# Optimization experiments

Hardware: AMD Instinct MI355X
Metric: run time of the kernel (lower is better)

The kernel has to match this reference:

```python
import jax, jax.numpy as jnp
import numpy as np

B, C, FS, Z_DIM, OUT_C, F_SIZE = 256, 512, 16, 64, 1, 3
NZ = FS * FS  # 256


def setup_inputs() -> dict:
    key = jax.random.key(0)
    k1, k2, k3, k4, k5 = jax.random.split(key, 5)
    # z: [B, C, H, W]
    z = jax.random.normal(k1, (B, C, FS, FS), dtype=jnp.float32)
    # 512 independent per-channel Linear(Nz -> z_dim): stacked weights/biases
    lim_in = 1.0 / np.sqrt(NZ)
    W_in = jax.random.uniform(k2, (C, NZ, Z_DIM), minval=-lim_in, maxval=lim_in, dtype=jnp.float32)
    b_in = jax.random.uniform(k3, (C, Z_DIM), minval=-lim_in, maxval=lim_in, dtype=jnp.float32)
    # shared Linear(z_dim -> out_channels*f_size*f_size)
    lim_out = 1.0 / np.sqrt(Z_DIM)
    W_out = jax.random.uniform(k4, (Z_DIM, OUT_C * F_SIZE * F_SIZE), minval=-lim_out, maxval=lim_out, dtype=jnp.float32)
    b_out = jax.random.uniform(k5, (OUT_C * F_SIZE * F_SIZE,), minval=-lim_out, maxval=lim_out, dtype=jnp.float32)
    return {"z": z, "W_in": W_in, "b_in": b_in, "W_out": W_out, "b_out": b_out}


def reference(z, W_in, b_in, W_out, b_out):
    batch = z.shape[0]
    # flatten each channel's HxW map: [B, C, Nz]
    x = z.reshape(batch, C, NZ)
    # per-channel Linear as one batched GEMM: [B, C, z_dim]
    a = jnp.einsum('bcn,cnz->bcz', x, W_in) + b_in[None, :, :]
    # shared output Linear: [B, C, out_c*f*f]
    k = jnp.einsum('bcz,zk->bck', a, W_out) + b_out
    # [B, C, out_channels, f_size, f_size]
    return k.reshape(batch, C, OUT_C, F_SIZE, F_SIZE)
```

## Files before the change

kernel.cpp:

```cpp
#include <hip/hip_runtime.h>

#define BB 256
#define CC 512
#define NZ 256
#define ZD 64
#define KK 9

template<int CTRL>
__device__ __forceinline__ float dpp_add(float v) {
    int o = __builtin_amdgcn_update_dpp(0, __float_as_int(v), CTRL, 0xF, 0xF, true);
    return v + __int_as_float(o);
}
__device__ __forceinline__ float red8(float v) {
    v = dpp_add<0xB1>(v);
    v = dpp_add<0x4E>(v);
    v = dpp_add<0x141>(v);
    return v;
}

__global__ __launch_bounds__(512, 2)
void hyper_kernel(const float* __restrict__ z,
                  const float* __restrict__ W_in,
                  const float* __restrict__ b_in,
                  const float* __restrict__ W_out,
                  const float* __restrict__ b_out,
                  float* __restrict__ out) {
    __shared__ __align__(16) float s_wfT[KK * NZ];
    __shared__ __align__(16) float s_woutT[KK * ZD];
    __shared__ float s_bin[ZD];
    __shared__ float s_biask[KK];

    const int c = blockIdx.x;
    const int t = threadIdx.x;

    for (int i = t; i < KK * ZD; i += 512) {
        float v = W_out[i];
        int zz = i / KK, k = i - zz * KK;
        s_woutT[k * ZD + zz] = v;
    }
    if (t < ZD) s_bin[t] = b_in[c * ZD + t];
    __syncthreads();

    {
        const int n = t >> 1, half = t & 1;
        const float* wrow = W_in + ((size_t)c * NZ + n) * ZD + half * 32;
        float acc[KK];
#pragma unroll
        for (int k = 0; k < KK; ++k) acc[k] = 0.f;
#pragma unroll
        for (int j = 0; j < 8; ++j) {
            const float4 w = *reinterpret_cast<const float4*>(wrow + 4 * j);
#pragma unroll
            for (int k = 0; k < KK; ++k) {
                const float4 wo = *reinterpret_cast<const float4*>(
                    &s_woutT[k * ZD + half * 32 + 4 * j]);
                acc[k] += w.x * wo.x + w.y * wo.y + w.z * wo.z + w.w * wo.w;
            }
        }
#pragma unroll
        for (int k = 0; k < KK; ++k) acc[k] = dpp_add<0xB1>(acc[k]);
        if (half == 0) {
#pragma unroll
            for (int k = 0; k < KK; ++k) s_wfT[k * NZ + n] = acc[k];
        }
        if (t < KK) {
            float s = 0.f;
            for (int zz = 0; zz < ZD; ++zz) s += s_bin[zz] * s_woutT[t * ZD + zz];
            s_biask[t] = s + b_out[t];
        }
    }
    __syncthreads();

    const int lane = t & 63;
    const int wave = t >> 6;
    const int g = lane >> 3;
    const int sub = lane & 7;
    const int b0 = wave * 32 + g * 4;
    const float biasS = s_biask[sub];
    const float bias8 = s_biask[8];

    const float* xp = z + ((size_t)b0 * CC + c) * NZ + sub * 4;
    const size_t bstr = (size_t)CC * NZ;

    float acc[4][KK];
#pragma unroll
    for (int bb = 0; bb < 4; ++bb)
#pragma unroll
        for (int k = 0; k < KK; ++k) acc[bb][k] = 0.f;

    float4 xb[2][4];
#pragma unroll
    for (int bb = 0; bb < 4; ++bb)
        xb[0][bb] = *reinterpret_cast<const float4*>(xp + bb * bstr);

#pragma unroll
    for (int j = 0; j < 8; ++j) {
        if (j < 7) {
#pragma unroll
            for (int bb = 0; bb < 4; ++bb)
                xb[(j + 1) & 1][bb] =
                    *reinterpret_cast<const float4*>(xp + bb * bstr + (j + 1) * 32);
        }
#pragma unroll
        for (int k = 0; k < KK; ++k) {
            const float4 wf = *reinterpret_cast<const float4*>(
                &s_wfT[k * NZ + sub * 4 + j * 32]);
#pragma unroll
            for (int bb = 0; bb < 4; ++bb) {
                const float4 x = xb[j & 1][bb];
                acc[bb][k] += x.x * wf.x + x.y * wf.y + x.z * wf.z + x.w * wf.w;
            }
        }
    }

#pragma unroll
    for (int bb = 0; bb < 4; ++bb)
#pragma unroll
        for (int k = 0; k < KK; ++k) acc[bb][k] = red8(acc[bb][k]);

#pragma unroll
    for (int bb = 0; bb < 4; ++bb) {
        float v = acc[bb][0];
#pragma unroll
        for (int k = 1; k < 8; ++k) {
            if (sub == k) v = acc[bb][k];
        }
        const size_t o0 = ((size_t)(b0 + bb) * CC + c) * KK;
        out[o0 + sub] = v + biasS;
        if (sub == 0) out[o0 + 8] = acc[bb][8] + bias8;
    }
}

extern "C" void kernel_launch(void* const* d_in, const int* in_sizes, int n_in,
                              void* d_out, int out_size, void* d_ws, size_t ws_size,
                              hipStream_t stream) {
    const float* z     = (const float*)d_in[0];
    const float* W_in  = (const float*)d_in[1];
    const float* b_in  = (const float*)d_in[2];
    const float* W_out = (const float*)d_in[3];
    const float* b_out = (const float*)d_in[4];
    float* out = (float*)d_out;
    hyper_kernel<<<dim3(CC), dim3(512), 0, stream>>>(z, W_in, b_in, W_out, b_out, out);
}
```

Baseline: 228.3 us.

## Split fused weight folding into separate kernel and double output-kernel grid

The fused W_in·W_out weights and per-channel biases are now computed by a separate kernel and written to workspace. A second kernel then runs a 512x2 grid of 256-thread blocks, each covering half the batch, instead of 512 blocks of 512 threads. It also deepens register prefetch of z to three buffers. The aim is more blocks for better latency hiding and load balance, at the cost of an extra launch and a workspace round trip of about 4.7 MB. The old fused kernel stays as a fallback when the workspace is too small.

```diff
diff --git a/kernel.cpp b/kernel.cpp
--- a/kernel.cpp
+++ b/kernel.cpp
@@ -16,6 +16,138 @@
     v = dpp_add<0x4E>(v);
     v = dpp_add<0x141>(v);
     return v;
+}
+
+__global__ __launch_bounds__(512, 2)
+void wf_kernel(const float* __restrict__ W_in,
+               const float* __restrict__ b_in,
+               const float* __restrict__ W_out,
+               const float* __restrict__ b_out,
+               float* __restrict__ wf,
+               float* __restrict__ bk) {
+    __shared__ __align__(16) float s_woutT[KK * ZD];
+    __shared__ float s_bin[ZD];
+
+    const int c = blockIdx.x;
+    const int t = threadIdx.x;
+
+    for (int i = t; i < KK * ZD; i += 512) {
+        float v = W_out[i];
+        int zz = i / KK, k = i - zz * KK;
+        s_woutT[k * ZD + zz] = v;
+    }
+    if (t < ZD) s_bin[t] = b_in[c * ZD + t];
+    __syncthreads();
+
+    const int n = t >> 1, half = t & 1;
+    const float* wrow = W_in + ((size_t)c * NZ + n) * ZD + half * 32;
+    float acc[KK];
+#pragma unroll
+    for (int k = 0; k < KK; ++k) acc[k] = 0.f;
+#pragma unroll
+    for (int j = 0; j < 8; ++j) {
+        const float4 w = *reinterpret_cast<const float4*>(wrow + 4 * j);
+#pragma unroll
+        for (int k = 0; k < KK; ++k) {
+            const float4 wo = *reinterpret_cast<const float4*>(
+                &s_woutT[k * ZD + half * 32 + 4 * j]);
+            acc[k] += w.x * wo.x + w.y * wo.y + w.z * wo.z + w.w * wo.w;
+        }
+    }
+#pragma unroll
+    for (int k = 0; k < KK; ++k) acc[k] = dpp_add<0xB1>(acc[k]);
+    if (half == 0) {
+#pragma unroll
+        for (int k = 0; k < KK; ++k) wf[((size_t)c * KK + k) * NZ + n] = acc[k];
+    }
+    if (t < KK) {
+        float s = 0.f;
+        for (int zz = 0; zz < ZD; ++zz) s += s_bin[zz] * s_woutT[t * ZD + zz];
+        bk[c * KK + t] = s + b_out[t];
+    }
+}
+
+__global__ __launch_bounds__(256, 2)
+void out_kernel(const float* __restrict__ z,
+                const float* __restrict__ wf,
+                const float* __restrict__ bk,
+                float* __restrict__ out) {
+    __shared__ __align__(16) float s_wfT[KK * NZ];
+    __shared__ float s_biask[KK];
+
+    const int c = blockIdx.x;
+    const int bh = blockIdx.y;
+    const int t = threadIdx.x;
+
+    {
+        const float4* src = reinterpret_cast<const float4*>(wf + (size_t)c * KK * NZ);
+        float4* dst = reinterpret_cast<float4*>(s_wfT);
+        for (int i = t; i < KK * NZ / 4; i += 256) dst[i] = src[i];
+        if (t < KK) s_biask[t] = bk[c * KK + t];
+    }
+    __syncthreads();
+
+    const int lane = t & 63;
+    const int wave = t >> 6;
+    const int g = lane >> 3;
+    const int sub = lane & 7;
+    const int b0 = bh * 128 + wave * 32 + g * 4;
+    const float biasS = s_biask[sub];
+    const float bias8 = s_biask[8];
+
+    const float* xp = z + ((size_t)b0 * CC + c) * NZ + sub * 4;
+    const size_t bstr = (size_t)CC * NZ;
+
+    float acc[4][KK];
+#pragma unroll
+    for (int bb = 0; bb < 4; ++bb)
+#pragma unroll
+        for (int k = 0; k < KK; ++k) acc[bb][k] = 0.f;
+
+    float4 xb[3][4];
+#pragma unroll
+    for (int bb = 0; bb < 4; ++bb)
+        xb[0][bb] = *reinterpret_cast<const float4*>(xp + bb * bstr);
+#pragma unroll
+    for (int bb = 0; bb < 4; ++bb)
+        xb[1][bb] = *reinterpret_cast<const float4*>(xp + bb * bstr + 32);
+
+#pragma unroll
+    for (int j = 0; j < 8; ++j) {
+        if (j < 6) {
+#pragma unroll
+            for (int bb = 0; bb < 4; ++bb)
+                xb[(j + 2) % 3][bb] =
+                    *reinterpret_cast<const float4*>(xp + bb * bstr + (j + 2) * 32);
+        }
+#pragma unroll
+        for (int k = 0; k < KK; ++k) {
+            const float4 wfv = *reinterpret_cast<const float4*>(
+                &s_wfT[k * NZ + sub * 4 + j * 32]);
+#pragma unroll
+            for (int bb = 0; bb < 4; ++bb) {
+                const float4 x = xb[j % 3][bb];
+                acc[bb][k] += x.x * wfv.x + x.y * wfv.y + x.z * wfv.z + x.w * wfv.w;
+            }
+        }
+    }
+
+#pragma unroll
+    for (int bb = 0; bb < 4; ++bb)
+#pragma unroll
+        for (int k = 0; k < KK; ++k) acc[bb][k] = red8(acc[bb][k]);
+
+#pragma unroll
+    for (int bb = 0; bb < 4; ++bb) {
+        float v = acc[bb][0];
+#pragma unroll
+        for (int k = 1; k < 8; ++k) {
+            if (sub == k) v = acc[bb][k];
+        }
+        const size_t o0 = ((size_t)(b0 + bb) * CC + c) * KK;
+        out[o0 + sub] = v + biasS;
+        if (sub == 0) out[o0 + 8] = acc[bb][8] + bias8;
+    }
 }
 
 __global__ __launch_bounds__(512, 2)
@@ -103,12 +235,12 @@
         }
 #pragma unroll
         for (int k = 0; k < KK; ++k) {
-            const float4 wf = *reinterpret_cast<const float4*>(
+            const float4 wfv = *reinterpret_cast<const float4*>(
                 &s_wfT[k * NZ + sub * 4 + j * 32]);
 #pragma unroll
             for (int bb = 0; bb < 4; ++bb) {
                 const float4 x = xb[j & 1][bb];
-                acc[bb][k] += x.x * wf.x + x.y * wf.y + x.z * wf.z + x.w * wf.w;
+                acc[bb][k] += x.x * wfv.x + x.y * wfv.y + x.z * wfv.z + x.w * wfv.w;
             }
         }
     }
@@ -140,5 +272,17 @@
     const float* W_out = (const float*)d_in[3];
     const float* b_out = (const float*)d_in[4];
     float* out = (float*)d_out;
-    hyper_kernel<<<dim3(CC), dim3(512), 0, stream>>>(z, W_in, b_in, W_out, b_out, out);
-}
+
+    const size_t WF_ELTS = (size_t)CC * KK * NZ;
+    const size_t BK_ELTS = (size_t)CC * KK;
+    const size_t NEED = (WF_ELTS + BK_ELTS) * sizeof(float);
+
+    if (d_ws != nullptr && ws_size >= NEED) {
+        float* wf = (float*)d_ws;
+        float* bk = wf + WF_ELTS;
+        wf_kernel<<<dim3(CC), dim3(512), 0, stream>>>(W_in, b_in, W_out, b_out, wf, bk);
+        out_kernel<<<dim3(CC, 2), dim3(256), 0, stream>>>(z, wf, bk, out);
+    } else {
+        hyper_kernel<<<dim3(CC), dim3(512), 0, stream>>>(z, W_in, b_in, W_out, b_out, out);
+    }
+}
```

Measured after the change: 232.5 us. No clear change (+1.9%).
